# Performance work log

Hardware: AMD Instinct MI355X
Metric: run time of the kernel (lower is better)

## Reference

```python
import jax, jax.numpy as jnp
import numpy as np

H = 56; W = 56; WS = 7; NW = WS * WS  # 49 tokens per window
HEADS = 8; DIM = 256; HIDDEN = 4 * DIM
SHIFT = NW // 2  # gilbert shift = 24 (shift_size > 0)
SCALE = (DIM // HEADS) ** -0.5
EPS = 1e-5


def _sgn(v):
    return -1 if v < 0 else 1 if v > 0 else 0


def _generate2d(x, y, ax, ay, bx, by, result):
    w = abs(ax + ay); h = abs(bx + by)
    dax, day = _sgn(ax), _sgn(ay); dbx, dby = _sgn(bx), _sgn(by)
    if h == 1 or w == 1:
        if h == 1:
            for _ in range(w):
                result.append((x, y)); x, y = x + dax, y + day
        elif w == 1:
            for _ in range(h):
                result.append((x, y)); x, y = x + dbx, y + dby
        return
    ax2, ay2 = ax // 2, ay // 2; bx2, by2 = bx // 2, by // 2
    w2 = abs(ax2 + ay2); h2 = abs(bx2 + by2)
    if 2 * w > 3 * h:
        if w2 % 2 and w > 2:
            ax2, ay2 = ax2 + dax, ay2 + day
        _generate2d(x, y, ax2, ay2, bx, by, result)
        _generate2d(x + ax2, y + ay2, ax - ax2, ay - ay2, bx, by, result)
    else:
        if h2 % 2 and h > 2:
            bx2, by2 = bx2 + dbx, by2 + dby
        _generate2d(x, y, bx2, by2, ax2, ay2, result)
        _generate2d(x + bx2, y + by2, ax, ay, bx - bx2, by - by2, result)
        _generate2d(x + (ax - dax) + (bx2 - dbx), y + (ay - day) + (by2 - dby),
                    -bx2, -by2, -(ax - ax2), -(ay - ay2), result)


def _gilbert2d(width, height):
    result = []
    if width >= height:
        _generate2d(0, 0, width, 0, 0, height, result)
    else:
        _generate2d(0, 0, 0, height, width, 0, result)
    return result


def _make_rel_index():
    # reverse_map[idx] = (y, x) for gilbert position idx
    path = _gilbert2d(W, H)
    rev = np.zeros((H * W, 2), dtype=np.int64)
    for i, (px, py) in enumerate(path[:H * W]):
        rev[i, 0] = py; rev[i, 1] = px
    pos = np.roll(rev, SHIFT, axis=0)  # shifted block: roll positions by ws^2//2
    n_windows = (H * W) // NW
    pos = pos[:n_windows * NW].reshape(n_windows, NW, 2)
    dh = pos[:, :, 0][:, :, None] - pos[:, :, 0][:, None, :] + (H - 1)
    dw = pos[:, :, 1][:, :, None] - pos[:, :, 1][:, None, :] + (W - 1)
    return (dh * (2 * W - 1) + dw).astype(np.int32)  # (nW, 49, 49)


def setup_inputs() -> dict:
    key = jax.random.key(0)
    ks = jax.random.split(key, 8)
    B, L, C = 32, H * W, DIM
    return {
        "x": jax.random.normal(ks[0], (B, L, C), jnp.float32),
        "qkv_w": jax.random.normal(ks[1], (C, 3 * C), jnp.float32) * 0.02,
        "qkv_b": jnp.zeros((3 * C,), jnp.float32),
        "proj_w": jax.random.normal(ks[2], (C, C), jnp.float32) * 0.02,
        "proj_b": jnp.zeros((C,), jnp.float32),
        "bias_table": jax.random.normal(ks[3], ((2 * H - 1) * (2 * W - 1), HEADS), jnp.float32) * 0.02,
        "norm1_w": jnp.ones((C,), jnp.float32),
        "norm1_b": jnp.zeros((C,), jnp.float32),
        "norm2_w": jnp.ones((C,), jnp.float32),
        "norm2_b": jnp.zeros((C,), jnp.float32),
        "fc1_w": jax.random.normal(ks[4], (C, HIDDEN), jnp.float32) * 0.02,
        "fc1_b": jnp.zeros((HIDDEN,), jnp.float32),
        "fc2_w": jax.random.normal(ks[5], (HIDDEN, C), jnp.float32) * 0.02,
        "fc2_b": jnp.zeros((C,), jnp.float32),
        "rel_index": jnp.asarray(_make_rel_index()),
    }


def _layernorm(x, w, b):
    mu = jnp.mean(x, axis=-1, keepdims=True)
    var = jnp.mean(jnp.square(x - mu), axis=-1, keepdims=True)
    return (x - mu) * jax.lax.rsqrt(var + EPS) * w + b


def reference(x, qkv_w, qkv_b, proj_w, proj_b, bias_table,
              norm1_w, norm1_b, norm2_w, norm2_b,
              fc1_w, fc1_b, fc2_w, fc2_b, rel_index):
    B, L, C = x.shape
    n_win = L // NW
    hd = C // HEADS

    shortcut = x
    h = _layernorm(x, norm1_w, norm1_b)
    # gilbert forward shift along the curve, then window partition
    h = jnp.roll(h, SHIFT, axis=1)
    hw = h.reshape(B * n_win, NW, C)

    qkv = (hw @ qkv_w + qkv_b).reshape(B * n_win, NW, 3, HEADS, hd)
    qkv = jnp.transpose(qkv, (2, 0, 3, 1, 4))  # (3, B*nW, heads, N, hd)
    q, k, v = qkv[0] * SCALE, qkv[1], qkv[2]

    attn = jnp.einsum('bhnd,bhmd->bhnm', q, k)  # (B*nW, heads, 49, 49)
    bias = jnp.transpose(bias_table[rel_index], (0, 3, 1, 2))  # (nW, heads, 49, 49)
    attn = attn.reshape(B, n_win, HEADS, NW, NW) + bias[None]
    attn = jax.nn.softmax(attn, axis=-1).reshape(B * n_win, HEADS, NW, NW)

    out = jnp.einsum('bhnm,bhmd->bhnd', attn, v)
    out = jnp.transpose(out, (0, 2, 1, 3)).reshape(B * n_win, NW, C)
    out = out @ proj_w + proj_b

    # window merge + gilbert reverse shift
    out = out.reshape(B, L, C)
    out = jnp.roll(out, -SHIFT, axis=1)

    x = shortcut + out
    h2 = _layernorm(x, norm2_w, norm2_b)
    h2 = jax.nn.gelu(h2 @ fc1_w + fc1_b, approximate=False) @ fc2_w + fc2_b
    return x + h2
```

## Files before the change

kernel.cpp:

```cpp
#include <hip/hip_runtime.h>
#include <math.h>

typedef unsigned short u16;
typedef __attribute__((ext_vector_type(8))) short bfrag;
typedef __attribute__((ext_vector_type(4))) float f32x4;
typedef __attribute__((ext_vector_type(4))) unsigned short us4;

#define B_SZ 32
#define L_SZ 3136
#define C_SZ 256
#define NHEADS 8
#define HID_SZ 1024
#define NW 49
#define NWIN 64
#define SHIFT 24
#define M_SZ (B_SZ * L_SZ)
#define SCALEF 0.17677669529663687f

__device__ __forceinline__ float bf2f(u16 u) {
  union { unsigned int i; float f; } v; v.i = ((unsigned)u) << 16; return v.f;
}
__device__ __forceinline__ u16 f2bf(float f) {
  union { unsigned int i; float f; } v; v.f = f;
  return (u16)((v.i + 0x7fffu + ((v.i >> 16) & 1u)) >> 16);
}
__device__ __forceinline__ void gload_lds16(const u16* g, u16* l) {
  __builtin_amdgcn_global_load_lds(
      (const __attribute__((address_space(1))) unsigned int*)g,
      (__attribute__((address_space(3))) unsigned int*)l, 16, 0, 0);
}

__global__ void transpose_kernel(const float* __restrict__ in, u16* __restrict__ out,
                                 int K, int N) {
  const int idx = blockIdx.x * 256 + threadIdx.x;
  if (idx >= K * N) return;
  const int n = idx / K;
  const int k = idx - n * K;
  out[idx] = f2bf(in[(size_t)k * N + n]);
}

__global__ void bias_kernel(const float* __restrict__ tab, const int* __restrict__ rel,
                            float* __restrict__ bm) {
  const int idx = blockIdx.x * 256 + threadIdx.x;
  const int tot = NWIN * NHEADS * NW * NW;
  if (idx >= tot) return;
  const int w = idx / (NHEADS * NW * NW);
  const int r = idx - w * (NHEADS * NW * NW);
  const int h = r / (NW * NW);
  const int ij = r - h * (NW * NW);
  bm[idx] = tab[(size_t)rel[w * NW * NW + ij] * NHEADS + h];
}

__global__ __launch_bounds__(256) void ln1_kernel(
    const float* __restrict__ x, const float* __restrict__ w,
    const float* __restrict__ b, u16* __restrict__ out) {
  const int wv = threadIdx.x >> 6;
  const int lane = threadIdx.x & 63;
  const int row0 = blockIdx.x * 16 + wv * 4;
  float4 u[4];
#pragma unroll
  for (int r = 0; r < 4; ++r)
    u[r] = *((const float4*)x + (size_t)(row0 + r) * 64 + lane);
  float s[4], sq[4];
#pragma unroll
  for (int r = 0; r < 4; ++r) {
    s[r]  = u[r].x + u[r].y + u[r].z + u[r].w;
    sq[r] = u[r].x * u[r].x + u[r].y * u[r].y + u[r].z * u[r].z + u[r].w * u[r].w;
  }
#pragma unroll
  for (int d = 1; d < 64; d <<= 1)
#pragma unroll
    for (int r = 0; r < 4; ++r) {
      s[r] += __shfl_xor(s[r], d); sq[r] += __shfl_xor(sq[r], d);
    }
  float wv4[4], bv4[4];
#pragma unroll
  for (int j = 0; j < 4; ++j) { wv4[j] = w[lane * 4 + j]; bv4[j] = b[lane * 4 + j]; }
#pragma unroll
  for (int r = 0; r < 4; ++r) {
    const int row = row0 + r;
    const float mu = s[r] * (1.0f / C_SZ);
    const float rs = rsqrtf(sq[r] * (1.0f / C_SZ) - mu * mu + 1e-5f);
    const int bb = row / L_SZ;
    int l2 = row - bb * L_SZ + SHIFT;
    if (l2 >= L_SZ) l2 -= L_SZ;
    const float vv[4] = {u[r].x, u[r].y, u[r].z, u[r].w};
    us4 ov;
#pragma unroll
    for (int j = 0; j < 4; ++j) ov[j] = f2bf((vv[j] - mu) * rs * wv4[j] + bv4[j]);
    *(us4*)(out + ((size_t)bb * L_SZ + l2) * C_SZ + lane * 4) = ov;
  }
}

__global__ __launch_bounds__(256) void ln2_kernel(
    const u16* __restrict__ x, const float* __restrict__ w,
    const float* __restrict__ b, u16* __restrict__ out) {
  const int wv = threadIdx.x >> 6;
  const int lane = threadIdx.x & 63;
  const int row0 = blockIdx.x * 16 + wv * 4;
  us4 u[4];
#pragma unroll
  for (int r = 0; r < 4; ++r)
    u[r] = *(const us4*)(x + (size_t)(row0 + r) * C_SZ + lane * 4);
  float v[4][4], s[4], sq[4];
#pragma unroll
  for (int r = 0; r < 4; ++r) {
    s[r] = 0.f; sq[r] = 0.f;
#pragma unroll
    for (int j = 0; j < 4; ++j) {
      v[r][j] = bf2f(u[r][j]); s[r] += v[r][j]; sq[r] += v[r][j] * v[r][j];
    }
  }
#pragma unroll
  for (int d = 1; d < 64; d <<= 1)
#pragma unroll
    for (int r = 0; r < 4; ++r) {
      s[r] += __shfl_xor(s[r], d); sq[r] += __shfl_xor(sq[r], d);
    }
  float wv4[4], bv4[4];
#pragma unroll
  for (int j = 0; j < 4; ++j) { wv4[j] = w[lane * 4 + j]; bv4[j] = b[lane * 4 + j]; }
#pragma unroll
  for (int r = 0; r < 4; ++r) {
    const float mu = s[r] * (1.0f / C_SZ);
    const float rs = rsqrtf(sq[r] * (1.0f / C_SZ) - mu * mu + 1e-5f);
    us4 ov;
#pragma unroll
    for (int j = 0; j < 4; ++j) ov[j] = f2bf((v[r][j] - mu) * rs * wv4[j] + bv4[j]);
    *(us4*)(out + (size_t)(row0 + r) * C_SZ + lane * 4) = ov;
  }
}

#define BM 128
#define BN 128
#define BKT 64

template <int MODE>
__global__ __launch_bounds__(256, 2) void gemm_kernel(
    const u16* __restrict__ A, const u16* __restrict__ Bt,
    const float* __restrict__ bias, int N, int K, void* __restrict__ Cout,
    const float* __restrict__ resx, const u16* __restrict__ resb2) {
  __shared__ u16 Als[BM * BKT];
  __shared__ u16 Bls[BN * BKT];
  const int tid = threadIdx.x;
  const int lane = tid & 63;
  const int lr = lane & 15;
  const int lg = lane >> 4;
  const int m0 = blockIdx.y * BM;
  const int n0 = blockIdx.x * BN;
  const int wid = tid >> 6;
  const int wm = (wid >> 1) * 64;
  const int wn = (wid & 1) * 64;

  const int grow = lane >> 3;
  const int gch = (lane & 7) ^ grow;

  const f32x4 fzero = {0.f, 0.f, 0.f, 0.f};
  f32x4 acc[4][4];
#pragma unroll
  for (int i = 0; i < 4; ++i)
#pragma unroll
    for (int j = 0; j < 4; ++j) acc[i][j] = fzero;

  const u16* Agl = A + (size_t)m0 * K + gch * 8;
  const u16* Bgl = Bt + (size_t)n0 * K + gch * 8;

  for (int k0 = 0; k0 < K; k0 += BKT) {
#pragma unroll
    for (int g = 0; g < 4; ++g) {
      const int rbase = wid * 32 + g * 8;
      gload_lds16(Agl + (size_t)(rbase + grow) * K + k0, Als + rbase * 64);
      gload_lds16(Bgl + (size_t)(rbase + grow) * K + k0, Bls + rbase * 64);
    }
    __syncthreads();
#pragma unroll
    for (int s = 0; s < 2; ++s) {
      const int kg = s * 4 + lg;
      bfrag af[4], bfv[4];
#pragma unroll
      for (int m = 0; m < 4; ++m) {
        const int r = wm + m * 16 + lr;
        af[m] = *(const bfrag*)(Als + r * 64 + ((kg ^ (r & 7)) * 8));
      }
#pragma unroll
      for (int n = 0; n < 4; ++n) {
        const int r = wn + n * 16 + lr;
        bfv[n] = *(const bfrag*)(Bls + r * 64 + ((kg ^ (r & 7)) * 8));
      }
#pragma unroll
      for (int m = 0; m < 4; ++m)
#pragma unroll
        for (int n = 0; n < 4; ++n)
          acc[m][n] = __builtin_amdgcn_mfma_f32_16x16x32_bf16(af[m], bfv[n],
                                                              acc[m][n], 0, 0, 0);
    }
    __syncthreads();
  }

  float bv4[4];
#pragma unroll
  for (int n = 0; n < 4; ++n) bv4[n] = bias[n0 + wn + n * 16 + lr];

#pragma unroll
  for (int m = 0; m < 4; ++m) {
#pragma unroll
    for (int i = 0; i < 4; ++i) {
      const int row = m0 + wm + m * 16 + lg * 4 + i;
      if (MODE == 1) {
        const int bb = row / L_SZ;
        int l2 = row - bb * L_SZ - SHIFT;
        if (l2 < 0) l2 += L_SZ;
        const size_t orow = (size_t)bb * L_SZ + l2;
#pragma unroll
        for (int n = 0; n < 4; ++n) {
          const int col = n0 + wn + n * 16 + lr;
          ((u16*)Cout)[orow * N + col] =
              f2bf(resx[orow * N + col] + acc[m][n][i] + bv4[n]);
        }
      } else {
#pragma unroll
        for (int n = 0; n < 4; ++n) {
          const int col = n0 + wn + n * 16 + lr;
          float v = acc[m][n][i] + bv4[n];
          if (MODE == 2) v = 0.5f * v * (1.0f + erff(v * 0.70710678f));
          if (MODE == 3) {
            v += bf2f(resb2[(size_t)row * N + col]);
            ((float*)Cout)[(size_t)row * N + col] = v;
          } else {
            ((u16*)Cout)[(size_t)row * N + col] = f2bf(v);
          }
        }
      }
    }
  }
}

__global__ __launch_bounds__(256) void attn_kernel(const u16* __restrict__ qkv,
                                                   const float* __restrict__ bm,
                                                   u16* __restrict__ out, int widx0) {
  __shared__ u16 Pls[4][64 * 72];
  const int wl = blockIdx.x;
  const int w = (widx0 + wl) & (NWIN - 1);
  const int wv = threadIdx.x >> 6;
  const int lane = threadIdx.x & 63;
  const int lr = lane & 15;
  const int lg = lane >> 4;
  const size_t base = (size_t)wl * NW;
  u16* P = Pls[wv];
  const f32x4 fzero = {0.f, 0.f, 0.f, 0.f};

  for (int rep = 0; rep < 2; ++rep) {
    const int h = wv * 2 + rep;
    bfrag qf[4], kf[4];
#pragma unroll
    for (int m = 0; m < 4; ++m) {
      int r = m * 16 + lr; if (r > NW - 1) r = NW - 1;
      qf[m] = *(const bfrag*)(qkv + (base + r) * 768 + h * 32 + lg * 8);
      kf[m] = *(const bfrag*)(qkv + (base + r) * 768 + 256 + h * 32 + lg * 8);
    }
    f32x4 s[4][4];
#pragma unroll
    for (int m = 0; m < 4; ++m)
#pragma unroll
      for (int n = 0; n < 4; ++n)
        s[m][n] = __builtin_amdgcn_mfma_f32_16x16x32_bf16(qf[m], kf[n], fzero, 0, 0, 0);

    const float* bh = bm + (size_t)(w * NHEADS + h) * (NW * NW);
#pragma unroll
    for (int m = 0; m < 4; ++m) {
#pragma unroll
      for (int i = 0; i < 4; ++i) {
        const int row = m * 16 + lg * 4 + i;
        const int brow = row > NW - 1 ? NW - 1 : row;
        float vals[4];
#pragma unroll
        for (int n = 0; n < 4; ++n) {
          const int c = n * 16 + lr;
          vals[n] = (c < NW) ? (s[m][n][i] * SCALEF + bh[brow * NW + c]) : -1e30f;
        }
        float mx = fmaxf(fmaxf(vals[0], vals[1]), fmaxf(vals[2], vals[3]));
#pragma unroll
        for (int d = 1; d < 16; d <<= 1) mx = fmaxf(mx, __shfl_xor(mx, d));
        float sum = 0.f;
#pragma unroll
        for (int n = 0; n < 4; ++n) { vals[n] = __expf(vals[n] - mx); sum += vals[n]; }
#pragma unroll
        for (int d = 1; d < 16; d <<= 1) sum += __shfl_xor(sum, d);
        const float inv = 1.0f / sum;
#pragma unroll
        for (int n = 0; n < 4; ++n)
          P[row * 72 + n * 16 + lr] = f2bf(vals[n] * inv);
      }
    }
    f32x4 o[4][2];
#pragma unroll
    for (int m = 0; m < 4; ++m) { o[m][0] = fzero; o[m][1] = fzero; }
#pragma unroll
    for (int s2 = 0; s2 < 2; ++s2) {
      bfrag pf[4];
#pragma unroll
      for (int m = 0; m < 4; ++m)
        pf[m] = *(const bfrag*)(P + (m * 16 + lr) * 72 + s2 * 32 + lg * 8);
#pragma unroll
      for (int n = 0; n < 2; ++n) {
        bfrag vf;
#pragma unroll
        for (int i = 0; i < 8; ++i) {
          int kk = s2 * 32 + lg * 8 + i; if (kk > NW - 1) kk = NW - 1;
          vf[i] = *(const short*)(qkv + (base + kk) * 768 + 512 + h * 32 + n * 16 + lr);
        }
#pragma unroll
        for (int m = 0; m < 4; ++m)
          o[m][n] = __builtin_amdgcn_mfma_f32_16x16x32_bf16(pf[m], vf, o[m][n], 0, 0, 0);
      }
    }
#pragma unroll
    for (int m = 0; m < 4; ++m)
#pragma unroll
      for (int i = 0; i < 4; ++i) {
        const int row = m * 16 + lg * 4 + i;
        if (row < NW) {
#pragma unroll
          for (int n = 0; n < 2; ++n)
            out[(base + row) * C_SZ + h * 32 + n * 16 + lr] = f2bf(o[m][n][i]);
        }
      }
  }
}

extern "C" void kernel_launch(void* const* d_in, const int* in_sizes, int n_in,
                              void* d_out, int out_size, void* d_ws, size_t ws_size,
                              hipStream_t stream) {
  (void)in_sizes; (void)n_in; (void)out_size;
  const float* x     = (const float*)d_in[0];
  const float* qkvw  = (const float*)d_in[1];
  const float* qkvb  = (const float*)d_in[2];
  const float* projw = (const float*)d_in[3];
  const float* projb = (const float*)d_in[4];
  const float* btab  = (const float*)d_in[5];
  const float* n1w   = (const float*)d_in[6];
  const float* n1b   = (const float*)d_in[7];
  const float* n2w   = (const float*)d_in[8];
  const float* n2b   = (const float*)d_in[9];
  const float* fc1w  = (const float*)d_in[10];
  const float* fc1b  = (const float*)d_in[11];
  const float* fc2w  = (const float*)d_in[12];
  const float* fc2b  = (const float*)d_in[13];
  const int* rel     = (const int*)d_in[14];

  char* ws = (char*)d_ws;
  size_t off = 0;
  auto alloc = [&](size_t bytes) -> char* {
    char* p = ws + off; off += (bytes + 255) & ~(size_t)255; return p;
  };
  u16* qkvwT   = (u16*)alloc((size_t)768 * 256 * 2);
  u16* projwT  = (u16*)alloc((size_t)256 * 256 * 2);
  u16* fc1wT   = (u16*)alloc((size_t)1024 * 256 * 2);
  u16* fc2wT   = (u16*)alloc((size_t)256 * 1024 * 2);
  float* biasm = (float*)alloc((size_t)NWIN * NHEADS * NW * NW * 4);
  u16* bufh    = (u16*)alloc((size_t)M_SZ * C_SZ * 2);
  u16* x2b     = (u16*)alloc((size_t)M_SZ * C_SZ * 2);

  const size_t full_scr = (size_t)M_SZ * HID_SZ * 2;
  const int nch = (ws_size >= off + full_scr + 256) ? 1 : 4;
  const int mch = M_SZ / nch;
  const int wch = (B_SZ * NWIN) / nch;
  u16* scratch2 = (u16*)alloc((size_t)mch * HID_SZ * 2);

  transpose_kernel<<<(256 * 768 + 255) / 256, 256, 0, stream>>>(qkvw, qkvwT, 256, 768);
  transpose_kernel<<<(256 * 256 + 255) / 256, 256, 0, stream>>>(projw, projwT, 256, 256);
  transpose_kernel<<<(256 * 1024 + 255) / 256, 256, 0, stream>>>(fc1w, fc1wT, 256, 1024);
  transpose_kernel<<<(1024 * 256 + 255) / 256, 256, 0, stream>>>(fc2w, fc2wT, 1024, 256);
  bias_kernel<<<(NWIN * NHEADS * NW * NW + 255) / 256, 256, 0, stream>>>(btab, rel, biasm);

  ln1_kernel<<<M_SZ / 16, 256, 0, stream>>>(x, n1w, n1b, bufh);

  for (int c = 0; c < nch; ++c) {
    const size_t roff = (size_t)c * mch;
    gemm_kernel<0><<<dim3(768 / BN, mch / BM), 256, 0, stream>>>(
        bufh + roff * C_SZ, qkvwT, qkvb, 768, 256, scratch2, nullptr, nullptr);
    attn_kernel<<<wch, 256, 0, stream>>>(scratch2, biasm, bufh + roff * C_SZ, c * wch);
  }

  gemm_kernel<1><<<dim3(256 / BN, M_SZ / BM), 256, 0, stream>>>(
      bufh, projwT, projb, 256, 256, x2b, x, nullptr);

  for (int q = 0; q < nch; ++q) {
    const size_t roff = (size_t)q * mch;
    ln2_kernel<<<mch / 16, 256, 0, stream>>>(x2b + roff * C_SZ, n2w, n2b,
                                             bufh + roff * C_SZ);
    gemm_kernel<2><<<dim3(1024 / BN, mch / BM), 256, 0, stream>>>(
        bufh + roff * C_SZ, fc1wT, fc1b, 1024, 256, scratch2, nullptr, nullptr);
    gemm_kernel<3><<<dim3(256 / BN, mch / BM), 256, 0, stream>>>(
        scratch2, fc2wT, fc2b, 256, 1024, (float*)d_out + roff * C_SZ,
        nullptr, x2b + roff * C_SZ);
  }
}
```

Baseline: 511.1 us.

## Fuse LN2+FC1+GELU+FC2 into one MLP kernel and pre-transpose V for attention

```diff
diff --git a/kernel.cpp b/kernel.cpp
--- a/kernel.cpp
+++ b/kernel.cpp
@@ -92,45 +92,6 @@
   }
 }
 
-__global__ __launch_bounds__(256) void ln2_kernel(
-    const u16* __restrict__ x, const float* __restrict__ w,
-    const float* __restrict__ b, u16* __restrict__ out) {
-  const int wv = threadIdx.x >> 6;
-  const int lane = threadIdx.x & 63;
-  const int row0 = blockIdx.x * 16 + wv * 4;
-  us4 u[4];
-#pragma unroll
-  for (int r = 0; r < 4; ++r)
-    u[r] = *(const us4*)(x + (size_t)(row0 + r) * C_SZ + lane * 4);
-  float v[4][4], s[4], sq[4];
-#pragma unroll
-  for (int r = 0; r < 4; ++r) {
-    s[r] = 0.f; sq[r] = 0.f;
-#pragma unroll
-    for (int j = 0; j < 4; ++j) {
-      v[r][j] = bf2f(u[r][j]); s[r] += v[r][j]; sq[r] += v[r][j] * v[r][j];
-    }
-  }
-#pragma unroll
-  for (int d = 1; d < 64; d <<= 1)
-#pragma unroll
-    for (int r = 0; r < 4; ++r) {
-      s[r] += __shfl_xor(s[r], d); sq[r] += __shfl_xor(sq[r], d);
-    }
-  float wv4[4], bv4[4];
-#pragma unroll
-  for (int j = 0; j < 4; ++j) { wv4[j] = w[lane * 4 + j]; bv4[j] = b[lane * 4 + j]; }
-#pragma unroll
-  for (int r = 0; r < 4; ++r) {
-    const float mu = s[r] * (1.0f / C_SZ);
-    const float rs = rsqrtf(sq[r] * (1.0f / C_SZ) - mu * mu + 1e-5f);
-    us4 ov;
-#pragma unroll
-    for (int j = 0; j < 4; ++j) ov[j] = f2bf((v[r][j] - mu) * rs * wv4[j] + bv4[j]);
-    *(us4*)(out + (size_t)(row0 + r) * C_SZ + lane * 4) = ov;
-  }
-}
-
 #define BM 128
 #define BN 128
 #define BKT 64
@@ -139,7 +100,7 @@
 __global__ __launch_bounds__(256, 2) void gemm_kernel(
     const u16* __restrict__ A, const u16* __restrict__ Bt,
     const float* __restrict__ bias, int N, int K, void* __restrict__ Cout,
-    const float* __restrict__ resx, const u16* __restrict__ resb2) {
+    const float* __restrict__ resx, u16* __restrict__ vt) {
   __shared__ u16 Als[BM * BKT];
   __shared__ u16 Bls[BN * BKT];
   const int tid = threadIdx.x;
@@ -218,16 +179,22 @@
               f2bf(resx[orow * N + col] + acc[m][n][i] + bv4[n]);
         }
       } else {
-#pragma unroll
-        for (int n = 0; n < 4; ++n) {
-          const int col = n0 + wn + n * 16 + lr;
-          float v = acc[m][n][i] + bv4[n];
-          if (MODE == 2) v = 0.5f * v * (1.0f + erff(v * 0.70710678f));
-          if (MODE == 3) {
-            v += bf2f(resb2[(size_t)row * N + col]);
-            ((float*)Cout)[(size_t)row * N + col] = v;
-          } else {
-            ((u16*)Cout)[(size_t)row * N + col] = f2bf(v);
+        if (n0 + wn < 512) {
+#pragma unroll
+          for (int n = 0; n < 4; ++n) {
+            const int col = n0 + wn + n * 16 + lr;
+            ((u16*)Cout)[(size_t)row * 512 + col] = f2bf(acc[m][n][i] + bv4[n]);
+          }
+        } else {
+          const unsigned widx = (unsigned)row / 49u;
+          const int kk = row - (int)widx * 49;
+#pragma unroll
+          for (int n = 0; n < 4; ++n) {
+            const int col = n0 + wn + n * 16 + lr - 512;
+            const int hh = col >> 5;
+            const int d = col & 31;
+            vt[(((size_t)widx * NHEADS + hh) * 32 + d) * 64 + kk] =
+                f2bf(acc[m][n][i] + bv4[n]);
           }
         }
       }
@@ -235,17 +202,18 @@
   }
 }
 
-__global__ __launch_bounds__(256) void attn_kernel(const u16* __restrict__ qkv,
+__global__ __launch_bounds__(256) void attn_kernel(const u16* __restrict__ qk,
+                                                   const u16* __restrict__ vt,
                                                    const float* __restrict__ bm,
-                                                   u16* __restrict__ out, int widx0) {
+                                                   u16* __restrict__ out) {
   __shared__ u16 Pls[4][64 * 72];
-  const int wl = blockIdx.x;
-  const int w = (widx0 + wl) & (NWIN - 1);
+  const int widx = blockIdx.x;
+  const int w = widx & (NWIN - 1);
   const int wv = threadIdx.x >> 6;
   const int lane = threadIdx.x & 63;
   const int lr = lane & 15;
   const int lg = lane >> 4;
-  const size_t base = (size_t)wl * NW;
+  const size_t base = (size_t)widx * NW;
   u16* P = Pls[wv];
   const f32x4 fzero = {0.f, 0.f, 0.f, 0.f};
 
@@ -255,8 +223,8 @@
 #pragma unroll
     for (int m = 0; m < 4; ++m) {
       int r = m * 16 + lr; if (r > NW - 1) r = NW - 1;
-      qf[m] = *(const bfrag*)(qkv + (base + r) * 768 + h * 32 + lg * 8);
-      kf[m] = *(const bfrag*)(qkv + (base + r) * 768 + 256 + h * 32 + lg * 8);
+      qf[m] = *(const bfrag*)(qk + (base + r) * 512 + h * 32 + lg * 8);
+      kf[m] = *(const bfrag*)(qk + (base + r) * 512 + 256 + h * 32 + lg * 8);
     }
     f32x4 s[4][4];
 #pragma unroll
@@ -292,27 +260,25 @@
           P[row * 72 + n * 16 + lr] = f2bf(vals[n] * inv);
       }
     }
+    const u16* vth = vt + ((size_t)widx * NHEADS + h) * 32 * 64;
     f32x4 o[4][2];
 #pragma unroll
     for (int m = 0; m < 4; ++m) { o[m][0] = fzero; o[m][1] = fzero; }
 #pragma unroll
     for (int s2 = 0; s2 < 2; ++s2) {
-      bfrag pf[4];
+      bfrag pf[4], vf[2];
 #pragma unroll
       for (int m = 0; m < 4; ++m)
         pf[m] = *(const bfrag*)(P + (m * 16 + lr) * 72 + s2 * 32 + lg * 8);
 #pragma unroll
-      for (int n = 0; n < 2; ++n) {
-        bfrag vf;
-#pragma unroll
-        for (int i = 0; i < 8; ++i) {
-          int kk = s2 * 32 + lg * 8 + i; if (kk > NW - 1) kk = NW - 1;
-          vf[i] = *(const short*)(qkv + (base + kk) * 768 + 512 + h * 32 + n * 16 + lr);
-        }
-#pragma unroll
-        for (int m = 0; m < 4; ++m)
-          o[m][n] = __builtin_amdgcn_mfma_f32_16x16x32_bf16(pf[m], vf, o[m][n], 0, 0, 0);
-      }
+      for (int n = 0; n < 2; ++n)
+        vf[n] = *(const bfrag*)(vth + (size_t)(n * 16 + lr) * 64 + s2 * 32 + lg * 8);
+#pragma unroll
+      for (int m = 0; m < 4; ++m)
+#pragma unroll
+        for (int n = 0; n < 2; ++n)
+          o[m][n] = __builtin_amdgcn_mfma_f32_16x16x32_bf16(pf[m], vf[n],
+                                                            o[m][n], 0, 0, 0);
     }
 #pragma unroll
     for (int m = 0; m < 4; ++m)
@@ -328,10 +294,108 @@
   }
 }
 
+__global__ __launch_bounds__(256) void mlp_kernel(
+    const u16* __restrict__ x2b, const float* __restrict__ n2w,
+    const float* __restrict__ n2b, const u16* __restrict__ w1t,
+    const float* __restrict__ b1, const u16* __restrict__ w2t,
+    const float* __restrict__ b2, float* __restrict__ outp) {
+  __shared__ u16 As[64 * 256];
+  __shared__ u16 Hs[4][16 * 64];
+  const int wid = threadIdx.x >> 6;
+  const int lane = threadIdx.x & 63;
+  const int lr = lane & 15;
+  const int lg = lane >> 4;
+  const int m0 = blockIdx.x * 64;
+  const f32x4 fzero = {0.f, 0.f, 0.f, 0.f};
+
+#pragma unroll
+  for (int g = 0; g < 8; ++g) {
+    const int rl = wid * 16 + g * 2 + (lane >> 5);
+    const int sc = (lane & 31) ^ (rl & 7);
+    gload_lds16(x2b + (size_t)(m0 + rl) * 256 + sc * 8,
+                As + (wid * 16 + g * 2) * 256);
+  }
+  asm volatile("s_waitcnt vmcnt(0)" ::: "memory");
+
+  {
+    float wv4[4], bv4[4];
+#pragma unroll
+    for (int j = 0; j < 4; ++j) { wv4[j] = n2w[lane * 4 + j]; bv4[j] = n2b[lane * 4 + j]; }
+    for (int rr = 0; rr < 16; ++rr) {
+      const int r = wid * 16 + rr;
+      u16* ap = As + r * 256 + (((lane >> 1) ^ (r & 7)) << 3) + ((lane & 1) << 2);
+      us4 u = *(const us4*)ap;
+      float v[4]; float s = 0.f, sq = 0.f;
+#pragma unroll
+      for (int j = 0; j < 4; ++j) { v[j] = bf2f(u[j]); s += v[j]; sq += v[j] * v[j]; }
+#pragma unroll
+      for (int d = 1; d < 64; d <<= 1) { s += __shfl_xor(s, d); sq += __shfl_xor(sq, d); }
+      const float mu = s * (1.0f / C_SZ);
+      const float rs = rsqrtf(sq * (1.0f / C_SZ) - mu * mu + 1e-5f);
+      us4 ov;
+#pragma unroll
+      for (int j = 0; j < 4; ++j) ov[j] = f2bf((v[j] - mu) * rs * wv4[j] + bv4[j]);
+      *(us4*)ap = ov;
+    }
+  }
+
+  f32x4 acc2[16];
+#pragma unroll
+  for (int n = 0; n < 16; ++n) acc2[n] = fzero;
+  u16* H = Hs[wid];
+  const int arow = wid * 16 + lr;
+
+  for (int c = 0; c < 16; ++c) {
+    f32x4 acc1[4];
+#pragma unroll
+    for (int n = 0; n < 4; ++n) acc1[n] = fzero;
+#pragma unroll
+    for (int kt = 0; kt < 8; ++kt) {
+      const bfrag af = *(const bfrag*)(As + arow * 256 + (((kt * 4 + lg) ^ (arow & 7)) << 3));
+#pragma unroll
+      for (int nl = 0; nl < 4; ++nl) {
+        const bfrag bw = *(const bfrag*)(w1t + (size_t)(c * 64 + nl * 16 + lr) * 256 +
+                                         kt * 32 + lg * 8);
+        acc1[nl] = __builtin_amdgcn_mfma_f32_16x16x32_bf16(af, bw, acc1[nl], 0, 0, 0);
+      }
+    }
+#pragma unroll
+    for (int nl = 0; nl < 4; ++nl)
+#pragma unroll
+      for (int i = 0; i < 4; ++i) {
+        const int rl = lg * 4 + i;
+        const int col = nl * 16 + lr;
+        float v = acc1[nl][i] + b1[c * 64 + col];
+        v = 0.5f * v * (1.0f + erff(v * 0.70710678f));
+        H[rl * 64 + ((((col >> 3) ^ (rl & 7))) << 3) + (col & 7)] = f2bf(v);
+      }
+#pragma unroll
+    for (int kt2 = 0; kt2 < 2; ++kt2) {
+      const bfrag ah = *(const bfrag*)(H + lr * 64 + (((kt2 * 4 + lg) ^ (lr & 7)) << 3));
+#pragma unroll
+      for (int n2 = 0; n2 < 16; ++n2) {
+        const bfrag bw2 = *(const bfrag*)(w2t + (size_t)(n2 * 16 + lr) * 1024 +
+                                          c * 64 + kt2 * 32 + lg * 8);
+        acc2[n2] = __builtin_amdgcn_mfma_f32_16x16x32_bf16(ah, bw2, acc2[n2], 0, 0, 0);
+      }
+    }
+  }
+
+#pragma unroll
+  for (int n2 = 0; n2 < 16; ++n2)
+#pragma unroll
+    for (int i = 0; i < 4; ++i) {
+      const int row = m0 + wid * 16 + lg * 4 + i;
+      const int col = n2 * 16 + lr;
+      outp[(size_t)row * 256 + col] =
+          acc2[n2][i] + b2[col] + bf2f(x2b[(size_t)row * 256 + col]);
+    }
+}
+
 extern "C" void kernel_launch(void* const* d_in, const int* in_sizes, int n_in,
                               void* d_out, int out_size, void* d_ws, size_t ws_size,
                               hipStream_t stream) {
-  (void)in_sizes; (void)n_in; (void)out_size;
+  (void)in_sizes; (void)n_in; (void)out_size; (void)ws_size;
   const float* x     = (const float*)d_in[0];
   const float* qkvw  = (const float*)d_in[1];
   const float* qkvb  = (const float*)d_in[2];
@@ -360,12 +424,8 @@
   float* biasm = (float*)alloc((size_t)NWIN * NHEADS * NW * NW * 4);
   u16* bufh    = (u16*)alloc((size_t)M_SZ * C_SZ * 2);
   u16* x2b     = (u16*)alloc((size_t)M_SZ * C_SZ * 2);
-
-  const size_t full_scr = (size_t)M_SZ * HID_SZ * 2;
-  const int nch = (ws_size >= off + full_scr + 256) ? 1 : 4;
-  const int mch = M_SZ / nch;
-  const int wch = (B_SZ * NWIN) / nch;
-  u16* scratch2 = (u16*)alloc((size_t)mch * HID_SZ * 2);
+  u16* qkbuf   = (u16*)alloc((size_t)M_SZ * 512 * 2);
+  u16* vtbuf   = (u16*)alloc((size_t)B_SZ * NWIN * NHEADS * 32 * 64 * 2);
 
   transpose_kernel<<<(256 * 768 + 255) / 256, 256, 0, stream>>>(qkvw, qkvwT, 256, 768);
   transpose_kernel<<<(256 * 256 + 255) / 256, 256, 0, stream>>>(projw, projwT, 256, 256);
@@ -375,24 +435,14 @@
 
   ln1_kernel<<<M_SZ / 16, 256, 0, stream>>>(x, n1w, n1b, bufh);
 
-  for (int c = 0; c < nch; ++c) {
-    const size_t roff = (size_t)c * mch;
-    gemm_kernel<0><<<dim3(768 / BN, mch / BM), 256, 0, stream>>>(
-        bufh + roff * C_SZ, qkvwT, qkvb, 768, 256, scratch2, nullptr, nullptr);
-    attn_kernel<<<wch, 256, 0, stream>>>(scratch2, biasm, bufh + roff * C_SZ, c * wch);
-  }
+  gemm_kernel<0><<<dim3(768 / BN, M_SZ / BM), 256, 0, stream>>>(
+      bufh, qkvwT, qkvb, 768, 256, qkbuf, nullptr, vtbuf);
+
+  attn_kernel<<<B_SZ * NWIN, 256, 0, stream>>>(qkbuf, vtbuf, biasm, bufh);
 
   gemm_kernel<1><<<dim3(256 / BN, M_SZ / BM), 256, 0, stream>>>(
       bufh, projwT, projb, 256, 256, x2b, x, nullptr);
 
-  for (int q = 0; q < nch; ++q) {
-    const size_t roff = (size_t)q * mch;
-    ln2_kernel<<<mch / 16, 256, 0, stream>>>(x2b + roff * C_SZ, n2w, n2b,
-                                             bufh + roff * C_SZ);
-    gemm_kernel<2><<<dim3(1024 / BN, mch / BM), 256, 0, stream>>>(
-        bufh + roff * C_SZ, fc1wT, fc1b, 1024, 256, scratch2, nullptr, nullptr);
-    gemm_kernel<3><<<dim3(256 / BN, mch / BM), 256, 0, stream>>>(
-        scratch2, fc2wT, fc2b, 256, 1024, (float*)d_out + roff * C_SZ,
-        nullptr, x2b + roff * C_SZ);
-  }
-}
+  mlp_kernel<<<M_SZ / 64, 256, 0, stream>>>(x2b, n2w, n2b, fc1wT, fc1b,
+                                            fc2wT, fc2b, (float*)d_out);
+}
```

Result: slower. 1.283 ms (+151.0%).
